# Kernel optimization log

Hardware: AMD Instinct MI355X
Metric: run time of the kernel (lower is better)

The kernel has to match this reference:

```python
import jax, jax.numpy as jnp
import numpy as np

B, HEADS, T, QH, QW, D = 2, 8, 8, 16, 16, 64
KT, KH, KW = T, QH, QW  # key shape == query shape


def _rel_index(q_n, k_n):
    q_ratio = round(max(k_n / q_n, 1.0))
    k_ratio = round(max(q_n / k_n, 1.0))
    d = jnp.arange(q_n)[:, None] * q_ratio - jnp.arange(k_n)[None, :] * k_ratio
    return d + (k_n - 1) * k_ratio  # [q_n, k_n] indices into embedding table


def setup_inputs() -> dict:
    key = jax.random.key(0)
    k1, k2, k3, k4, k5 = jax.random.split(key, 5)
    query = jax.random.normal(k1, (B, HEADS, T * QH * QW, D), dtype=jnp.float32)
    scores = jax.random.normal(k2, (B, HEADS, T * QH * QW, KT * KH * KW), dtype=jnp.float32)
    height_emb = jax.random.normal(k3, (2 * (max(QH, KH) - 1) + 1, D), dtype=jnp.float32)
    width_emb = jax.random.normal(k4, (2 * (max(QW, KW) - 1) + 1, D), dtype=jnp.float32)
    time_emb = jax.random.normal(k5, (2 * (max(T, KT) - 1) + 1, D), dtype=jnp.float32)
    return {"query": query, "scores": scores, "height_emb": height_emb,
            "width_emb": width_emb, "time_emb": time_emb}


def reference(query, scores, height_emb, width_emb, time_emb):
    # gather relative-position embeddings (static indices)
    Rh = height_emb[_rel_index(QH, KH)]   # [qh, kh, D]
    Rw = width_emb[_rel_index(QW, KW)]    # [qw, kw, D]
    Rt = time_emb[_rel_index(T, KT)]      # [t,  kt, D]

    q = query.reshape(B, HEADS, T, QH, QW, D)
    rel_h = jnp.einsum('bNthwc,hkc->bNthwk', q, Rh)  # [B,N,T,qh,qw,kh]
    rel_w = jnp.einsum('bNthwc,wkc->bNthwk', q, Rw)  # [B,N,T,qh,qw,kw]
    rel_t = jnp.einsum('bNthwc,tkc->bNthwk', q, Rt)  # [B,N,T,qh,qw,kt]

    s = scores.reshape(B, HEADS, T, QH, QW, KT, KH, KW)
    s = s + rel_h[:, :, :, :, :, None, :, None]
    s = s + rel_w[:, :, :, :, :, None, None, :]
    s = s + rel_t[:, :, :, :, :, :, None, None]
    return s.reshape(B, HEADS, T * QH * QW, KT * KH * KW)
```

## Files before the change

### kernel.cpp

```cpp
#include <hip/hip_runtime.h>


#define ROWS 4

typedef float v4f __attribute__((ext_vector_type(4)));

__global__ __launch_bounds__(256, 8) void relpos_fused_v4(
    const float* __restrict__ query,
    const float* __restrict__ scores,
    const float* __restrict__ hemb,
    const float* __restrict__ wemb,
    const float* __restrict__ temb,
    float* __restrict__ out)
{
    __shared__ float biasH[ROWS][16];
    __shared__ float biasW[ROWS][16];
    __shared__ float biasT[ROWS][8];

    const int tid  = threadIdx.x;
    const int wv   = tid >> 6;
    const int lane = tid & 63;

    const int grow = blockIdx.x * ROWS + wv;
    const int row  = grow & 2047;
    const int tt   = row >> 8;
    const int qh   = (row >> 4) & 15;
    const int qw   = row & 15;

    if (lane < 40) {
        const float* emb;
        int eidx;
        if (lane < 16)      { emb = hemb; eidx = qh - lane + 15; }
        else if (lane < 32) { emb = wemb; eidx = qw - (lane - 16) + 15; }
        else                { emb = temb; eidx = tt - (lane - 32) + 7; }
        const v4f* e4 = (const v4f*)(emb + eidx * 64);
        const v4f* q4 = (const v4f*)(query + (size_t)grow * 64);
        v4f a4 = (v4f)(0.f);
        #pragma unroll
        for (int k = 0; k < 16; ++k) {
            a4 += q4[k] * e4[k];
        }
        const float acc = (a4.x + a4.y) + (a4.z + a4.w);
        if (lane < 16)      biasH[wv][lane] = acc;
        else if (lane < 32) biasW[wv][lane - 16] = acc;
        else                biasT[wv][lane - 32] = acc;
    }

    const float h  = biasH[wv][(lane >> 2) & 15];
    const v4f  w4  = ((const v4f*)biasW[wv])[lane & 3];
    const v4f  hw4 = w4 + h;
    float tv[8];
    #pragma unroll
    for (int i = 0; i < 8; ++i) tv[i] = biasT[wv][i];

    const v4f* s4p = (const v4f*)scores + (size_t)grow * 512 + lane;
    v4f*       o4p = (v4f*)out          + (size_t)grow * 512 + lane;

    v4f s[8];
    #pragma unroll
    for (int i = 0; i < 8; ++i)
        s[i] = __builtin_nontemporal_load(&s4p[i * 64]);
    #pragma unroll
    for (int i = 0; i < 8; ++i) {
        v4f o = s[i] + hw4 + tv[i];
        __builtin_nontemporal_store(o, &o4p[i * 64]);
    }
}

extern "C" void kernel_launch(void* const* d_in, const int* in_sizes, int n_in,
                              void* d_out, int out_size, void* d_ws, size_t ws_size,
                              hipStream_t stream) {
    const float* query  = (const float*)d_in[0];
    const float* scores = (const float*)d_in[1];
    const float* hemb   = (const float*)d_in[2];
    const float* wemb   = (const float*)d_in[3];
    const float* temb   = (const float*)d_in[4];
    float* out = (float*)d_out;

    relpos_fused_v4<<<32768 / ROWS, 256, 0, stream>>>(
        query, scores, hemb, wemb, temb, out);
}
```

Before: 105.2 us.

## Process eight rows per wave with double-buffered loads and shuffle-based bias broadcast

Each wave now handles eight query rows instead of one, loading the next row's scores into a second register buffer while the current row is biased and stored. Bias values are shared with wave shuffles instead of LDS, which removes the shared-memory round trip. The grid shrinks eightfold and the occupancy hint in launch bounds is dropped. The extra buffers raise register use, which could lower occupancy on a kernel bound by memory bandwidth.

New measurement: 119.3 us. 13.4% more time.

```diff
diff --git a/kernel.cpp b/kernel.cpp
--- a/kernel.cpp
+++ b/kernel.cpp
@@ -1,11 +1,12 @@
 #include <hip/hip_runtime.h>
 
 
-#define ROWS 4
-
 typedef float v4f __attribute__((ext_vector_type(4)));
 
-__global__ __launch_bounds__(256, 8) void relpos_fused_v4(
+#define WAVES 4
+#define RPW   8
+
+__global__ __launch_bounds__(256) void relpos_fused_v5(
     const float* __restrict__ query,
     const float* __restrict__ scores,
     const float* __restrict__ hemb,
@@ -13,57 +14,79 @@
     const float* __restrict__ temb,
     float* __restrict__ out)
 {
-    __shared__ float biasH[ROWS][16];
-    __shared__ float biasW[ROWS][16];
-    __shared__ float biasT[ROWS][8];
-
     const int tid  = threadIdx.x;
     const int wv   = tid >> 6;
     const int lane = tid & 63;
+    const int r0   = (blockIdx.x * WAVES + wv) * RPW;
 
-    const int grow = blockIdx.x * ROWS + wv;
-    const int row  = grow & 2047;
-    const int tt   = row >> 8;
-    const int qh   = (row >> 4) & 15;
-    const int qw   = row & 15;
+    const int hsrc = lane >> 2;
+    const int wsrc = 16 + (lane & 3) * 4;
 
-    if (lane < 40) {
-        const float* emb;
-        int eidx;
-        if (lane < 16)      { emb = hemb; eidx = qh - lane + 15; }
-        else if (lane < 32) { emb = wemb; eidx = qw - (lane - 16) + 15; }
-        else                { emb = temb; eidx = tt - (lane - 32) + 7; }
-        const v4f* e4 = (const v4f*)(emb + eidx * 64);
-        const v4f* q4 = (const v4f*)(query + (size_t)grow * 64);
-        v4f a4 = (v4f)(0.f);
+    auto issue_loads = [&](int grow, v4f (&buf)[8]) {
+        const v4f* sp = (const v4f*)scores + (size_t)grow * 512 + lane;
         #pragma unroll
-        for (int k = 0; k < 16; ++k) {
-            a4 += q4[k] * e4[k];
+        for (int i = 0; i < 8; ++i)
+            buf[i] = __builtin_nontemporal_load(&sp[i * 64]);
+    };
+
+    auto compute_bias = [&](int grow, v4f& hw4, float (&tv)[8]) {
+        const int row = grow & 2047;
+        const int tt  = row >> 8;
+        const int qh  = (row >> 4) & 15;
+        const int qw  = row & 15;
+        float acc = 0.f;
+        if (lane < 40) {
+            const float* emb;
+            int eidx;
+            if (lane < 16)      { emb = hemb; eidx = qh - lane + 15; }
+            else if (lane < 32) { emb = wemb; eidx = qw - (lane - 16) + 15; }
+            else                { emb = temb; eidx = tt - (lane - 32) + 7; }
+            const v4f* e4 = (const v4f*)(emb + eidx * 64);
+            const v4f* q4 = (const v4f*)(query + (size_t)grow * 64);
+            v4f a4 = (v4f)(0.f);
+            #pragma unroll
+            for (int k = 0; k < 16; ++k) a4 += q4[k] * e4[k];
+            acc = (a4.x + a4.y) + (a4.z + a4.w);
         }
-        const float acc = (a4.x + a4.y) + (a4.z + a4.w);
-        if (lane < 16)      biasH[wv][lane] = acc;
-        else if (lane < 32) biasW[wv][lane - 16] = acc;
-        else                biasT[wv][lane - 32] = acc;
-    }
+        const float h = __shfl(acc, hsrc, 64);
+        v4f w;
+        w.x = __shfl(acc, wsrc + 0, 64);
+        w.y = __shfl(acc, wsrc + 1, 64);
+        w.z = __shfl(acc, wsrc + 2, 64);
+        w.w = __shfl(acc, wsrc + 3, 64);
+        hw4 = w + h;
+        #pragma unroll
+        for (int i = 0; i < 8; ++i) tv[i] = __shfl(acc, 32 + i, 64);
+    };
 
-    const float h  = biasH[wv][(lane >> 2) & 15];
-    const v4f  w4  = ((const v4f*)biasW[wv])[lane & 3];
-    const v4f  hw4 = w4 + h;
-    float tv[8];
+    auto flush = [&](int grow, const v4f (&buf)[8], const v4f& hw4,
+                     const float (&tv)[8]) {
+        v4f* op = (v4f*)out + (size_t)grow * 512 + lane;
+        #pragma unroll
+        for (int i = 0; i < 8; ++i) {
+            v4f o = buf[i] + hw4 + tv[i];
+            __builtin_nontemporal_store(o, &op[i * 64]);
+        }
+    };
+
+    v4f   bufA[8], bufB[8];
+    v4f   hwA, hwB;
+    float tvA[8], tvB[8];
+
+    issue_loads(r0, bufA);
+    compute_bias(r0, hwA, tvA);
+
     #pragma unroll
-    for (int i = 0; i < 8; ++i) tv[i] = biasT[wv][i];
+    for (int rr = 0; rr < RPW; rr += 2) {
+        issue_loads(r0 + rr + 1, bufB);
+        compute_bias(r0 + rr + 1, hwB, tvB);
+        flush(r0 + rr, bufA, hwA, tvA);
 
-    const v4f* s4p = (const v4f*)scores + (size_t)grow * 512 + lane;
-    v4f*       o4p = (v4f*)out          + (size_t)grow * 512 + lane;
-
-    v4f s[8];
-    #pragma unroll
-    for (int i = 0; i < 8; ++i)
-        s[i] = __builtin_nontemporal_load(&s4p[i * 64]);
-    #pragma unroll
-    for (int i = 0; i < 8; ++i) {
-        v4f o = s[i] + hw4 + tv[i];
-        __builtin_nontemporal_store(o, &o4p[i * 64]);
+        if (rr + 2 < RPW) {
+            issue_loads(r0 + rr + 2, bufA);
+            compute_bias(r0 + rr + 2, hwA, tvA);
+        }
+        flush(r0 + rr + 1, bufB, hwB, tvB);
     }
 }
 
@@ -77,6 +100,6 @@
     const float* temb   = (const float*)d_in[4];
     float* out = (float*)d_out;
 
-    relpos_fused_v4<<<32768 / ROWS, 256, 0, stream>>>(
+    relpos_fused_v5<<<32768 / (WAVES * RPW), 256, 0, stream>>>(
         query, scores, hemb, wemb, temb, out);
 }
```
